# Optimization experiments

Hardware: AMD Instinct MI355X
Metric: run time of the kernel (lower is better)

Reference implementation:

```python
import jax, jax.numpy as jnp
import numpy as np
import math

D_MODEL = 1024
NUM_HEADS = 16
D_HEAD = D_MODEL // NUM_HEADS
SEQ = 2048
BATCH = 2
THETA = 10000.0
SCALE = 1.0 / math.sqrt(D_HEAD)


def rope_cos_sin(seq_len, d_head, theta):
    # freqs_cis equivalent: angles[t, j] = t * theta**(-2j/d_head)
    inv_freq = 1.0 / (theta ** (jnp.arange(0, d_head, 2, dtype=jnp.float32) / d_head))
    t = jnp.arange(seq_len, dtype=jnp.float32)
    ang = jnp.outer(t, inv_freq)  # [S, d_head//2]
    return jnp.cos(ang), jnp.sin(ang)


def apply_rope(x, cos, sin):
    # x: [B, S, H, Dh]; treat consecutive pairs as complex numbers
    B, S, H, Dh = x.shape
    xr = x.reshape(B, S, H, Dh // 2, 2)
    x0, x1 = xr[..., 0], xr[..., 1]
    c = cos[None, :, None, :]
    s = sin[None, :, None, :]
    out = jnp.stack([x0 * c - x1 * s, x0 * s + x1 * c], axis=-1)
    return out.reshape(B, S, H, Dh)


def setup_inputs() -> dict:
    key = jax.random.key(0)
    ks = jax.random.split(key, 9)
    w_std = 0.02
    return {
        "qkv": jax.random.normal(ks[0], (BATCH, SEQ, D_MODEL), jnp.float32),
        "Wq": jax.random.normal(ks[1], (D_MODEL, D_MODEL), jnp.float32) * w_std,
        "bq": jax.random.normal(ks[2], (D_MODEL,), jnp.float32) * w_std,
        "Wk": jax.random.normal(ks[3], (D_MODEL, D_MODEL), jnp.float32) * w_std,
        "bk": jax.random.normal(ks[4], (D_MODEL,), jnp.float32) * w_std,
        "Wv": jax.random.normal(ks[5], (D_MODEL, D_MODEL), jnp.float32) * w_std,
        "bv": jax.random.normal(ks[6], (D_MODEL,), jnp.float32) * w_std,
        "Wo": jax.random.normal(ks[7], (D_MODEL, D_MODEL), jnp.float32) * w_std,
        "bo": jax.random.normal(ks[8], (D_MODEL,), jnp.float32) * w_std,
    }


def reference(qkv, Wq, bq, Wk, bk, Wv, bv, Wo, bo):
    B, S, D = qkv.shape
    cos, sin = rope_cos_sin(S, D_HEAD, THETA)
    # torch Linear: y = x @ W.T + b
    q = (qkv @ Wq.T + bq).reshape(B, S, NUM_HEADS, D_HEAD)
    k = (qkv @ Wk.T + bk).reshape(B, S, NUM_HEADS, D_HEAD)
    v = (qkv @ Wv.T + bv).reshape(B, S, NUM_HEADS, D_HEAD)
    q = apply_rope(q, cos, sin)
    k = apply_rope(k, cos, sin)
    scores = jnp.einsum("bqhd,bkhd->bhqk", q, k) * SCALE
    causal = jnp.triu(jnp.ones((S, S), dtype=bool), k=1)
    scores = jnp.where(causal[None, None], -1e30, scores)
    attn = jax.nn.softmax(scores, axis=-1)
    out = jnp.einsum("bhqk,bkhd->bqhd", attn, v).reshape(B, S, D)
    return out @ Wo.T + bo
```

## Files before the change

kernel.cpp:

```cpp
#include <hip/hip_runtime.h>
#include <hip/hip_bf16.h>
#include <stdint.h>
#include <math.h>


typedef __bf16 bf16;
typedef __attribute__((ext_vector_type(4))) __bf16 bf16x4;
typedef __attribute__((ext_vector_type(8))) __bf16 bf16x8;
typedef __attribute__((ext_vector_type(4))) float f32x4;
typedef __attribute__((ext_vector_type(16))) float f32x16;
typedef __attribute__((ext_vector_type(4))) uint32_t u32x4;

#define SEQN 2048
#define DMOD 1024
#define NHEAD 16
#define DHEAD 64
#define MTOT 4096
#define VSTR 2080
#define QSCALE_LOG2E 0.18033688011112042f
#define DEFER_THR 8.0f

__device__ __forceinline__ void gload_lds16(const bf16* g, bf16* l) {
  __builtin_amdgcn_global_load_lds(
      (const __attribute__((address_space(1))) uint32_t*)g,
      (__attribute__((address_space(3))) uint32_t*)l,
      16, 0, 0);
}

__device__ __forceinline__ uint32_t cvtpk(float lo, float hi) {
  uint32_t r;
  asm("v_cvt_pk_bf16_f32 %0, %1, %2" : "=v"(r) : "v"(lo), "v"(hi));
  return r;
}

__global__ __launch_bounds__(256) void prep_kernel(
    const float* __restrict__ X,
    const float* __restrict__ Wq, const float* __restrict__ Wk,
    const float* __restrict__ Wv, const float* __restrict__ Wo,
    bf16* __restrict__ Xb, bf16* __restrict__ Wqb, bf16* __restrict__ Wkb,
    bf16* __restrict__ Wvb, bf16* __restrict__ Wob,
    float* __restrict__ ctab, float* __restrict__ stab)
{
  const int tid = blockIdx.x * blockDim.x + threadIdx.x;
  const int nth = gridDim.x * blockDim.x;

  const float4* X4 = (const float4*)X;
  for (int i = tid; i < MTOT * DMOD / 4; i += nth) {
    float4 v = X4[i];
    bf16x4 o = { (bf16)v.x, (bf16)v.y, (bf16)v.z, (bf16)v.w };
    *(bf16x4*)(Xb + (size_t)i * 4) = o;
  }
  const float4* q4 = (const float4*)Wq;
  const float4* k4 = (const float4*)Wk;
  const float4* v4 = (const float4*)Wv;
  const float4* o4 = (const float4*)Wo;
  for (int i = tid; i < DMOD * DMOD / 4; i += nth) {
    float4 a = q4[i];
    float4 b = k4[i];
    float4 c = v4[i];
    float4 d = o4[i];
    *(bf16x4*)(Wqb + (size_t)i * 4) = bf16x4{ (bf16)a.x, (bf16)a.y, (bf16)a.z, (bf16)a.w };
    *(bf16x4*)(Wkb + (size_t)i * 4) = bf16x4{ (bf16)b.x, (bf16)b.y, (bf16)b.z, (bf16)b.w };
    *(bf16x4*)(Wvb + (size_t)i * 4) = bf16x4{ (bf16)c.x, (bf16)c.y, (bf16)c.z, (bf16)c.w };
    *(bf16x4*)(Wob + (size_t)i * 4) = bf16x4{ (bf16)d.x, (bf16)d.y, (bf16)d.z, (bf16)d.w };
  }
  for (int i = tid; i < SEQN * 32; i += nth) {
    const int s = i >> 5, p = i & 31;
    const float invf = (float)pow(10000.0, -(double)p / 32.0);
    const float ang = (float)s * invf;
    float sv, cv;
    sincosf(ang, &sv, &cv);
    ctab[i] = cv;
    stab[i] = sv;
  }
}

__global__ __launch_bounds__(256) void gemm_qkv(
    const bf16* __restrict__ Xb,
    const bf16* __restrict__ Wqb, const bf16* __restrict__ Wkb, const bf16* __restrict__ Wvb,
    const float* __restrict__ bq, const float* __restrict__ bk, const float* __restrict__ bv,
    const float* __restrict__ ctab, const float* __restrict__ stab,
    bf16* __restrict__ Qb, bf16* __restrict__ Kb, bf16* __restrict__ Vtb)
{
  __shared__ bf16 sA[3][128 * 32];
  __shared__ bf16 sB[3][128 * 32];

  const int z = blockIdx.z;
  const bf16* Bm = (z == 0) ? Wqb : (z == 1) ? Wkb : Wvb;
  const float* bias = (z == 0) ? bq : (z == 1) ? bk : bv;

  const int t = threadIdx.x;
  const int lane = t & 63, l15 = lane & 15, g = lane >> 4;
  const int wave = t >> 6, wm = wave >> 1, wn = wave & 1;
  const int tileM = blockIdx.y * 128, tileN = blockIdx.x * 128;

  f32x4 acc[4][4] = {};

  const bf16* gA = Xb + (size_t)(tileM + (t >> 2)) * DMOD + (t & 3) * 8;
  const bf16* gB = Bm + (size_t)(tileN + (t >> 2)) * DMOD + (t & 3) * 8;

  auto stage = [&](int buf, int k0) {
    gload_lds16(gA + k0, &sA[buf][t * 8]);
    gload_lds16(gA + k0 + 64 * DMOD, &sA[buf][2048 + t * 8]);
    gload_lds16(gB + k0, &sB[buf][t * 8]);
    gload_lds16(gB + k0 + 64 * DMOD, &sB[buf][2048 + t * 8]);
  };

  stage(0, 0);
  stage(1, 32);

  const int NS = DMOD / 32;
  int cur = 0;
  for (int s = 0; s < NS; ++s) {
    if (s + 2 < NS) {
      int pf = cur + 2; if (pf >= 3) pf -= 3;
      stage(pf, (s + 2) * 32);
      asm volatile("s_waitcnt vmcnt(8)" ::: "memory");
    } else if (s + 1 < NS) {
      asm volatile("s_waitcnt vmcnt(4)" ::: "memory");
    } else {
      asm volatile("s_waitcnt vmcnt(0)" ::: "memory");
    }
    __builtin_amdgcn_s_barrier();
    asm volatile("" ::: "memory");

    const bf16* cA = sA[cur];
    const bf16* cB = sB[cur];
    bf16x8 af[4], bfr[4];
#pragma unroll
    for (int i = 0; i < 4; ++i)
      af[i] = *(const bf16x8*)(cA + (wm * 64 + i * 16 + l15) * 32 + g * 8);
#pragma unroll
    for (int j = 0; j < 4; ++j)
      bfr[j] = *(const bf16x8*)(cB + (wn * 64 + j * 16 + l15) * 32 + g * 8);
#pragma unroll
    for (int i = 0; i < 4; ++i)
#pragma unroll
      for (int j = 0; j < 4; ++j)
        acc[i][j] = __builtin_amdgcn_mfma_f32_16x16x32_bf16(af[i], bfr[j], acc[i][j], 0, 0, 0);

    asm volatile("" ::: "memory");
    __builtin_amdgcn_s_barrier();
    cur = (cur == 2) ? 0 : cur + 1;
  }

#pragma unroll
  for (int j = 0; j < 4; ++j) {
    const int col = tileN + wn * 64 + j * 16 + l15;
    const float bcol = bias[col];
    const int h = col >> 6, d = col & 63;
#pragma unroll
    for (int i = 0; i < 4; ++i) {
#pragma unroll
      for (int r = 0; r < 4; ++r) {
        const int row = tileM + wm * 64 + i * 16 + g * 4 + r;
        const int b = row >> 11, s = row & (SEQN - 1);
        const float v = acc[i][j][r] + bcol;
        if (z != 2) {
          const int pair = d >> 1;
          const float cv = ctab[s * 32 + pair];
          const float sv = stab[s * 32 + pair];
          const float partner = __shfl_xor(v, 1);
          float rv = (d & 1) ? (partner * sv + v * cv) : (v * cv - partner * sv);
          if (z == 0) rv *= QSCALE_LOG2E;
          bf16* dst = (z == 0) ? Qb : Kb;
          dst[(((size_t)(b * NHEAD + h)) * SEQN + s) * DHEAD + d] = (bf16)rv;
        } else {
          Vtb[(((size_t)(b * NHEAD + h)) * DHEAD + d) * VSTR + s] = (bf16)v;
        }
      }
    }
  }
}

__global__ __launch_bounds__(256) void attn_kernel(
    const bf16* __restrict__ Qb, const bf16* __restrict__ Kb,
    const bf16* __restrict__ Vt, bf16* __restrict__ AO)
{
  __shared__ float sMrg[2][64][35];

  const int t = threadIdx.x;
  const int lane = t & 63, l31 = lane & 31, hi = lane >> 5;
  const int wave = t >> 6;
  const int sb = wave >> 1;
  const int half = wave & 1;

  const int bid = blockIdx.x;
  const int bh = bid & 31;
  const int grp = bid >> 8;
  const int w = (bid >> 5) & 7;
  const int jq = (grp == 0) ? (31 - w) : (grp == 1) ? (16 + w)
               : (grp == 2) ? (15 - w) : w;
  const int qbase = (2 * jq + sb) * 32;
  const int qg = qbase + l31;
  const int n = jq + 1;
  const int nA = (n + 1) >> 1;
  const int kv_lo = half ? nA : 0;
  const int kv_hi = half ? n : nA;

  const bf16* Kp = Kb + (size_t)bh * SEQN * DHEAD;
  const bf16* Vp = Vt + (size_t)bh * DHEAD * VSTR;
  const bf16* Qp = Qb + (size_t)bh * SEQN * DHEAD;
  const int b = bh >> 4, h = bh & 15;

  auto loadK = [&](bf16x8 (&K)[2][4], int kv0) {
#pragma unroll
    for (int s = 0; s < 2; ++s)
#pragma unroll
      for (int ch = 0; ch < 4; ++ch)
        K[s][ch] = *(const bf16x8*)(Kp + (size_t)(kv0 + 32 * s + l31) * DHEAD + 16 * ch + 8 * hi);
  };
  auto loadV = [&](bf16x8 (&V)[2][4], int kv0) {
#pragma unroll
    for (int dblk = 0; dblk < 2; ++dblk)
#pragma unroll
      for (int c = 0; c < 4; ++c)
        V[dblk][c] = *(const bf16x8*)(Vp + (size_t)(dblk * 32 + l31) * VSTR + kv0 + 16 * c + 8 * hi);
  };

  bf16x8 qf[4];
#pragma unroll
  for (int ch = 0; ch < 4; ++ch)
    qf[ch] = *(const bf16x8*)(Qp + (size_t)qg * DHEAD + 16 * ch + 8 * hi);

  f32x16 a0 = {}, a1 = {};
  float m = -1e30f, l = 0.f;

  if (kv_lo < kv_hi) {
    bf16x8 K[2][4], V[2][4];
    loadK(K, kv_lo * 64);
    loadV(V, kv_lo * 64);

    for (int it = kv_lo; it < kv_hi; ++it) {
      const int kv0 = it * 64;

      f32x16 s0 = {}, s1 = {};
      __builtin_amdgcn_s_setprio(1);
#pragma unroll
      for (int ch = 0; ch < 4; ++ch) {
        s0 = __builtin_amdgcn_mfma_f32_32x32x16_bf16(K[0][ch], qf[ch], s0, 0, 0, 0);
        s1 = __builtin_amdgcn_mfma_f32_32x32x16_bf16(K[1][ch], qf[ch], s1, 0, 0, 0);
      }
      __builtin_amdgcn_s_setprio(0);
      if (it + 1 < kv_hi) loadK(K, kv0 + 64);

      float tv[32];
#pragma unroll
      for (int i = 0; i < 16; ++i) { tv[i] = s0[i]; tv[16 + i] = s1[i]; }

      if (kv0 + 63 > qbase) {
#pragma unroll
        for (int i = 0; i < 32; ++i) {
          const int key = kv0 + 32 * (i >> 4) + ((i & 3) + 8 * ((i >> 2) & 3) + 4 * hi);
          if (key > qg) tv[i] = -1e30f;
        }
      }

      float red[16];
#pragma unroll
      for (int i = 0; i < 16; ++i) red[i] = fmaxf(tv[i], tv[i + 16]);
#pragma unroll
      for (int st = 8; st >= 1; st >>= 1)
#pragma unroll
        for (int i = 0; i < st; ++i) red[i] = fmaxf(red[i], red[i + st]);
      const float tmax_own = red[0];

      if (__any(tmax_own > m + DEFER_THR)) {
        const float tfull = fmaxf(tmax_own, __shfl_xor(tmax_own, 32));
        const float mnew = fmaxf(m, tfull);
        const float alpha = __builtin_amdgcn_exp2f(m - mnew);
        m = mnew;
        l *= alpha;
#pragma unroll
        for (int i = 0; i < 16; ++i) { a0[i] *= alpha; a1[i] *= alpha; }
      }

#pragma unroll
      for (int i = 0; i < 32; ++i) tv[i] = __builtin_amdgcn_exp2f(tv[i] - m);
#pragma unroll
      for (int i = 0; i < 16; ++i) red[i] = tv[i] + tv[i + 16];
#pragma unroll
      for (int st = 8; st >= 1; st >>= 1)
#pragma unroll
        for (int i = 0; i < st; ++i) red[i] += red[i + st];
      l += red[0];

      __builtin_amdgcn_s_setprio(1);
#pragma unroll
      for (int c = 0; c < 4; ++c) {
        const int b0 = (c & 1) * 8 + (c >> 1) * 16;
        const uint32_t P0  = cvtpk(tv[b0 + 0], tv[b0 + 1]);
        const uint32_t P0b = cvtpk(tv[b0 + 2], tv[b0 + 3]);
        const uint32_t P1  = cvtpk(tv[b0 + 4], tv[b0 + 5]);
        const uint32_t P1b = cvtpk(tv[b0 + 6], tv[b0 + 7]);
        const uint32_t sP0  = (uint32_t)__shfl_xor((int)P0, 32);
        const uint32_t sP0b = (uint32_t)__shfl_xor((int)P0b, 32);
        const uint32_t sP1  = (uint32_t)__shfl_xor((int)P1, 32);
        const uint32_t sP1b = (uint32_t)__shfl_xor((int)P1b, 32);
        u32x4 pw;
        pw[0] = hi ? sP1  : P0;
        pw[1] = hi ? sP1b : P0b;
        pw[2] = hi ? P1   : sP0;
        pw[3] = hi ? P1b  : sP0b;
        const bf16x8 pf = __builtin_bit_cast(bf16x8, pw);
        a0 = __builtin_amdgcn_mfma_f32_32x32x16_bf16(V[0][c], pf, a0, 0, 0, 0);
        a1 = __builtin_amdgcn_mfma_f32_32x32x16_bf16(V[1][c], pf, a1, 0, 0, 0);
      }
      __builtin_amdgcn_s_setprio(0);
      if (it + 1 < kv_hi) loadV(V, kv0 + 64);
    }
  }

  const float l_full = l + __shfl_xor(l, 32);

  if (half) {
#pragma unroll
    for (int i = 0; i < 16; ++i) {
      sMrg[sb][lane][i] = a0[i];
      sMrg[sb][lane][16 + i] = a1[i];
    }
    sMrg[sb][lane][32] = m;
    sMrg[sb][lane][33] = l_full;
  }
  __syncthreads();
  if (!half) {
    const float mB = sMrg[sb][lane][32];
    const float lB = sMrg[sb][lane][33];
    const float ms = fmaxf(m, mB);
    const float fA = __builtin_amdgcn_exp2f(m - ms);
    const float fB = __builtin_amdgcn_exp2f(mB - ms);
    const float linv = 1.f / (l_full * fA + lB * fB);
    const size_t rowoff = ((size_t)(b * SEQN + qg)) * DMOD + h * DHEAD;
#pragma unroll
    for (int dblk = 0; dblk < 2; ++dblk) {
      const f32x16& av = dblk ? a1 : a0;
#pragma unroll
      for (int rg = 0; rg < 4; ++rg) {
        const int d0 = dblk * 32 + rg * 8 + 4 * hi;
        bf16x4 ov;
#pragma unroll
        for (int e = 0; e < 4; ++e)
          ov[e] = (bf16)((av[rg * 4 + e] * fA + sMrg[sb][lane][dblk * 16 + rg * 4 + e] * fB) * linv);
        *(bf16x4*)(AO + rowoff + d0) = ov;
      }
    }
  }
}

__global__ __launch_bounds__(256) void gemm_out(
    const bf16* __restrict__ AO, const bf16* __restrict__ Wob,
    const float* __restrict__ bo, float* __restrict__ out)
{
  __shared__ bf16 sA[3][128 * 32];
  __shared__ bf16 sB[3][128 * 32];

  const int t = threadIdx.x;
  const int lane = t & 63, l15 = lane & 15, g = lane >> 4;
  const int wave = t >> 6, wm = wave >> 1, wn = wave & 1;
  const int tileM = blockIdx.y * 128, tileN = blockIdx.x * 128;

  f32x4 acc[4][4] = {};

  const bf16* gA = AO + (size_t)(tileM + (t >> 2)) * DMOD + (t & 3) * 8;
  const bf16* gB = Wob + (size_t)(tileN + (t >> 2)) * DMOD + (t & 3) * 8;

  auto stage = [&](int buf, int k0) {
    gload_lds16(gA + k0, &sA[buf][t * 8]);
    gload_lds16(gA + k0 + 64 * DMOD, &sA[buf][2048 + t * 8]);
    gload_lds16(gB + k0, &sB[buf][t * 8]);
    gload_lds16(gB + k0 + 64 * DMOD, &sB[buf][2048 + t * 8]);
  };

  stage(0, 0);
  stage(1, 32);

  const int NS = DMOD / 32;
  int cur = 0;
  for (int s = 0; s < NS; ++s) {
    if (s + 2 < NS) {
      int pf = cur + 2; if (pf >= 3) pf -= 3;
      stage(pf, (s + 2) * 32);
      asm volatile("s_waitcnt vmcnt(8)" ::: "memory");
    } else if (s + 1 < NS) {
      asm volatile("s_waitcnt vmcnt(4)" ::: "memory");
    } else {
      asm volatile("s_waitcnt vmcnt(0)" ::: "memory");
    }
    __builtin_amdgcn_s_barrier();
    asm volatile("" ::: "memory");

    const bf16* cA = sA[cur];
    const bf16* cB = sB[cur];
    bf16x8 af[4], bfr[4];
#pragma unroll
    for (int i = 0; i < 4; ++i)
      af[i] = *(const bf16x8*)(cA + (wm * 64 + i * 16 + l15) * 32 + g * 8);
#pragma unroll
    for (int j = 0; j < 4; ++j)
      bfr[j] = *(const bf16x8*)(cB + (wn * 64 + j * 16 + l15) * 32 + g * 8);
#pragma unroll
    for (int i = 0; i < 4; ++i)
#pragma unroll
      for (int j = 0; j < 4; ++j)
        acc[i][j] = __builtin_amdgcn_mfma_f32_16x16x32_bf16(af[i], bfr[j], acc[i][j], 0, 0, 0);

    asm volatile("" ::: "memory");
    __builtin_amdgcn_s_barrier();
    cur = (cur == 2) ? 0 : cur + 1;
  }

#pragma unroll
  for (int j = 0; j < 4; ++j) {
    const int col = tileN + wn * 64 + j * 16 + l15;
    const float bcol = bo[col];
#pragma unroll
    for (int i = 0; i < 4; ++i)
#pragma unroll
      for (int r = 0; r < 4; ++r) {
        const int row = tileM + wm * 64 + i * 16 + g * 4 + r;
        out[(size_t)row * DMOD + col] = acc[i][j][r] + bcol;
      }
  }
}

extern "C" void kernel_launch(void* const* d_in, const int* in_sizes, int n_in,
                              void* d_out, int out_size, void* d_ws, size_t ws_size,
                              hipStream_t stream)
{
  (void)in_sizes; (void)n_in; (void)out_size; (void)ws_size;
  const float* X  = (const float*)d_in[0];
  const float* Wq = (const float*)d_in[1];
  const float* bq = (const float*)d_in[2];
  const float* Wk = (const float*)d_in[3];
  const float* bk = (const float*)d_in[4];
  const float* Wv = (const float*)d_in[5];
  const float* bv = (const float*)d_in[6];
  const float* Wo = (const float*)d_in[7];
  const float* bo = (const float*)d_in[8];

  char* ws = (char*)d_ws;
  float* ctab = (float*)(ws + 0);
  float* stab = (float*)(ws + 262144);
  bf16* Xb  = (bf16*)(ws + 524288);
  bf16* Wqb = (bf16*)(ws + 8912896);
  bf16* Wkb = (bf16*)(ws + 11010048);
  bf16* Wvb = (bf16*)(ws + 13107200);
  bf16* Wob = (bf16*)(ws + 15204352);
  bf16* Qb  = (bf16*)(ws + 17301504);
  bf16* Kb  = (bf16*)(ws + 25690112);
  bf16* Vtb = (bf16*)(ws + 34078720);
  bf16* AO  = (bf16*)(ws + 42598400);

  prep_kernel<<<1024, 256, 0, stream>>>(X, Wq, Wk, Wv, Wo, Xb, Wqb, Wkb, Wvb, Wob, ctab, stab);
  gemm_qkv<<<dim3(8, 32, 3), 256, 0, stream>>>(Xb, Wqb, Wkb, Wvb, bq, bk, bv, ctab, stab, Qb, Kb, Vtb);
  attn_kernel<<<1024, 256, 0, stream>>>(Qb, Kb, Vtb, AO);
  gemm_out<<<dim3(8, 32), 256, 0, stream>>>(AO, Wob, bo, (float*)d_out);
}
```

Before: 146.2 us.

## Shrink attention KV tile to 32 keys with exact per-subblock causal bound

Changes the attention inner loop from 64-key to 32-key steps. Each wave now stops at its own 32-row query subblock's causal limit instead of the 64-row pair's limit, which skips a masked half-tile on the diagonal. The P shuffle is cut from four shfl_xor to two per MFMA pair by pre-selecting the words to exchange, and the s_setprio hints are dropped. In exchange the loop runs twice as many iterations with half the MFMAs each, so fixed per-iteration costs (the max and sum reductions, the rescale check, and load latency) make up a larger share of the work.

Measured after the change: 144.0 us. No clear change (-1.5%).

```diff
diff --git a/kernel.cpp b/kernel.cpp
--- a/kernel.cpp
+++ b/kernel.cpp
@@ -193,29 +193,27 @@
                : (grp == 2) ? (15 - w) : w;
   const int qbase = (2 * jq + sb) * 32;
   const int qg = qbase + l31;
-  const int n = jq + 1;
-  const int nA = (n + 1) >> 1;
+  const int n32 = 2 * jq + sb + 1;
+  const int nA = (n32 + 1) >> 1;
   const int kv_lo = half ? nA : 0;
-  const int kv_hi = half ? n : nA;
+  const int kv_hi = half ? n32 : nA;
 
   const bf16* Kp = Kb + (size_t)bh * SEQN * DHEAD;
   const bf16* Vp = Vt + (size_t)bh * DHEAD * VSTR;
   const bf16* Qp = Qb + (size_t)bh * SEQN * DHEAD;
   const int b = bh >> 4, h = bh & 15;
 
-  auto loadK = [&](bf16x8 (&K)[2][4], int kv0) {
-#pragma unroll
-    for (int s = 0; s < 2; ++s)
-#pragma unroll
-      for (int ch = 0; ch < 4; ++ch)
-        K[s][ch] = *(const bf16x8*)(Kp + (size_t)(kv0 + 32 * s + l31) * DHEAD + 16 * ch + 8 * hi);
+  auto loadK = [&](bf16x8 (&K)[4], int kv0) {
+#pragma unroll
+    for (int ch = 0; ch < 4; ++ch)
+      K[ch] = *(const bf16x8*)(Kp + (size_t)(kv0 + l31) * DHEAD + 16 * ch + 8 * hi);
   };
-  auto loadV = [&](bf16x8 (&V)[2][4], int kv0) {
+  auto loadV = [&](bf16x8 (&V)[2][2], int kv0) {
 #pragma unroll
     for (int dblk = 0; dblk < 2; ++dblk)
 #pragma unroll
-      for (int c = 0; c < 4; ++c)
-        V[dblk][c] = *(const bf16x8*)(Vp + (size_t)(dblk * 32 + l31) * VSTR + kv0 + 16 * c + 8 * hi);
+      for (int kh = 0; kh < 2; ++kh)
+        V[dblk][kh] = *(const bf16x8*)(Vp + (size_t)(dblk * 32 + l31) * VSTR + kv0 + 16 * kh + 8 * hi);
   };
 
   bf16x8 qf[4];
@@ -227,40 +225,33 @@
   float m = -1e30f, l = 0.f;
 
   if (kv_lo < kv_hi) {
-    bf16x8 K[2][4], V[2][4];
-    loadK(K, kv_lo * 64);
-    loadV(V, kv_lo * 64);
+    bf16x8 K[4];
+    bf16x8 V[2][2];
+    loadK(K, kv_lo * 32);
+    loadV(V, kv_lo * 32);
 
     for (int it = kv_lo; it < kv_hi; ++it) {
-      const int kv0 = it * 64;
-
-      f32x16 s0 = {}, s1 = {};
-      __builtin_amdgcn_s_setprio(1);
-#pragma unroll
-      for (int ch = 0; ch < 4; ++ch) {
-        s0 = __builtin_amdgcn_mfma_f32_32x32x16_bf16(K[0][ch], qf[ch], s0, 0, 0, 0);
-        s1 = __builtin_amdgcn_mfma_f32_32x32x16_bf16(K[1][ch], qf[ch], s1, 0, 0, 0);
-      }
-      __builtin_amdgcn_s_setprio(0);
-      if (it + 1 < kv_hi) loadK(K, kv0 + 64);
-
-      float tv[32];
-#pragma unroll
-      for (int i = 0; i < 16; ++i) { tv[i] = s0[i]; tv[16 + i] = s1[i]; }
-
-      if (kv0 + 63 > qbase) {
-#pragma unroll
-        for (int i = 0; i < 32; ++i) {
-          const int key = kv0 + 32 * (i >> 4) + ((i & 3) + 8 * ((i >> 2) & 3) + 4 * hi);
-          if (key > qg) tv[i] = -1e30f;
+      const int kv0 = it * 32;
+
+      f32x16 sc = {};
+#pragma unroll
+      for (int ch = 0; ch < 4; ++ch)
+        sc = __builtin_amdgcn_mfma_f32_32x32x16_bf16(K[ch], qf[ch], sc, 0, 0, 0);
+      if (it + 1 < kv_hi) loadK(K, kv0 + 32);
+
+      if (kv0 + 31 > qbase) {
+#pragma unroll
+        for (int i = 0; i < 16; ++i) {
+          const int key = kv0 + (i & 3) + 8 * (i >> 2) + 4 * hi;
+          if (key > qg) sc[i] = -1e30f;
         }
       }
 
-      float red[16];
-#pragma unroll
-      for (int i = 0; i < 16; ++i) red[i] = fmaxf(tv[i], tv[i + 16]);
-#pragma unroll
-      for (int st = 8; st >= 1; st >>= 1)
+      float red[8];
+#pragma unroll
+      for (int i = 0; i < 8; ++i) red[i] = fmaxf(sc[i], sc[i + 8]);
+#pragma unroll
+      for (int st = 4; st >= 1; st >>= 1)
 #pragma unroll
         for (int i = 0; i < st; ++i) red[i] = fmaxf(red[i], red[i + st]);
       const float tmax_own = red[0];
@@ -276,38 +267,35 @@
       }
 
 #pragma unroll
-      for (int i = 0; i < 32; ++i) tv[i] = __builtin_amdgcn_exp2f(tv[i] - m);
-#pragma unroll
-      for (int i = 0; i < 16; ++i) red[i] = tv[i] + tv[i + 16];
-#pragma unroll
-      for (int st = 8; st >= 1; st >>= 1)
+      for (int i = 0; i < 16; ++i) sc[i] = __builtin_amdgcn_exp2f(sc[i] - m);
+#pragma unroll
+      for (int i = 0; i < 8; ++i) red[i] = sc[i] + sc[i + 8];
+#pragma unroll
+      for (int st = 4; st >= 1; st >>= 1)
 #pragma unroll
         for (int i = 0; i < st; ++i) red[i] += red[i + st];
       l += red[0];
 
-      __builtin_amdgcn_s_setprio(1);
-#pragma unroll
-      for (int c = 0; c < 4; ++c) {
-        const int b0 = (c & 1) * 8 + (c >> 1) * 16;
-        const uint32_t P0  = cvtpk(tv[b0 + 0], tv[b0 + 1]);
-        const uint32_t P0b = cvtpk(tv[b0 + 2], tv[b0 + 3]);
-        const uint32_t P1  = cvtpk(tv[b0 + 4], tv[b0 + 5]);
-        const uint32_t P1b = cvtpk(tv[b0 + 6], tv[b0 + 7]);
-        const uint32_t sP0  = (uint32_t)__shfl_xor((int)P0, 32);
-        const uint32_t sP0b = (uint32_t)__shfl_xor((int)P0b, 32);
-        const uint32_t sP1  = (uint32_t)__shfl_xor((int)P1, 32);
-        const uint32_t sP1b = (uint32_t)__shfl_xor((int)P1b, 32);
+#pragma unroll
+      for (int kh = 0; kh < 2; ++kh) {
+        const uint32_t W0 = cvtpk(sc[8 * kh + 0], sc[8 * kh + 1]);
+        const uint32_t W1 = cvtpk(sc[8 * kh + 2], sc[8 * kh + 3]);
+        const uint32_t W2 = cvtpk(sc[8 * kh + 4], sc[8 * kh + 5]);
+        const uint32_t W3 = cvtpk(sc[8 * kh + 6], sc[8 * kh + 7]);
+        const uint32_t s0w = hi ? W0 : W2;
+        const uint32_t s1w = hi ? W1 : W3;
+        const uint32_t x0 = (uint32_t)__shfl_xor((int)s0w, 32);
+        const uint32_t x1 = (uint32_t)__shfl_xor((int)s1w, 32);
         u32x4 pw;
-        pw[0] = hi ? sP1  : P0;
-        pw[1] = hi ? sP1b : P0b;
-        pw[2] = hi ? P1   : sP0;
-        pw[3] = hi ? P1b  : sP0b;
+        pw[0] = hi ? x0 : W0;
+        pw[1] = hi ? x1 : W1;
+        pw[2] = hi ? W2 : x0;
+        pw[3] = hi ? W3 : x1;
         const bf16x8 pf = __builtin_bit_cast(bf16x8, pw);
-        a0 = __builtin_amdgcn_mfma_f32_32x32x16_bf16(V[0][c], pf, a0, 0, 0, 0);
-        a1 = __builtin_amdgcn_mfma_f32_32x32x16_bf16(V[1][c], pf, a1, 0, 0, 0);
-      }
-      __builtin_amdgcn_s_setprio(0);
-      if (it + 1 < kv_hi) loadV(V, kv0 + 64);
+        a0 = __builtin_amdgcn_mfma_f32_32x32x16_bf16(V[0][kh], pf, a0, 0, 0, 0);
+        a1 = __builtin_amdgcn_mfma_f32_32x32x16_bf16(V[1][kh], pf, a1, 0, 0, 0);
+      }
+      if (it + 1 < kv_hi) loadV(V, kv0 + 32);
     }
   }
 
```
